# Kernel tuning notes

Measured on AMD Instinct MI355X. Metric: run time of the kernel, lower is better.

Reference implementation:

```python
import jax, jax.numpy as jnp
import numpy as np

ALPHA = 0.2  # LeakyReLU negative slope


def setup_inputs() -> dict:
    key = jax.random.key(0)
    k1, k2, k3 = jax.random.split(key, 3)
    B, N, F_IN, F_OUT = 8, 2048, 128, 64
    h = jax.random.normal(k1, (B, N, F_IN), dtype=jnp.float32)
    # nn.Linear(in, out, bias=False).weight is [out, in]; we store the transposed
    # matmul-ready form W: [F_IN, F_OUT].
    W = jax.random.normal(k2, (F_IN, F_OUT), dtype=jnp.float32) * 0.05
    # attn_fc: Linear(2*F_OUT, 1, bias=False) -> weight vector a: [2*F_OUT]
    a = jax.random.normal(k3, (2 * F_OUT,), dtype=jnp.float32) * 0.05
    return {"h": h, "W": W, "a": a}


def reference(h, W, a):
    # h: [B, N, F_in], W: [F_in, F_out], a: [2*F_out]
    F_out = W.shape[1]
    Wh = h @ W  # [B, N, F_out]
    # cat([Wh_i, Wh_j]) @ a == Wh_i @ a1 + Wh_j @ a2 -- identical math,
    # avoids materializing the [B, N, N, 2F] tensor.
    s_i = Wh @ a[:F_out]  # [B, N] contribution of row node i
    s_j = Wh @ a[F_out:]  # [B, N] contribution of col node j
    e = jax.nn.leaky_relu(s_i[:, :, None] + s_j[:, None, :], negative_slope=ALPHA)  # [B, N, N]
    attn = jax.nn.softmax(e, axis=-1)  # softmax over neighbors j
    h_prime = jnp.einsum('bij,bjf->bif', attn, Wh)  # [B, N, F_out]
    return h_prime.mean(axis=1)  # [B, F_out]
```

## Files before the change

### kernel.cpp

```cpp
#include <hip/hip_runtime.h>
#include <hip/hip_bf16.h>


#define B 8
#define N 2048
#define FIN 128
#define FOUT 64
#define ALPHA 0.2f
#define NSLICE 4
#define SLICE (N / NSLICE)
#define GSLICE 16

__global__ __launch_bounds__(256) void k2_uv(const float* __restrict__ h,
                                             const float* __restrict__ W,
                                             const float* __restrict__ a,
                                             float* __restrict__ u, float* __restrict__ v) {
    __shared__ float sw[2 * FIN];
    int t = threadIdx.x;
    if (t < FIN) {
        float wa = 0.f, wb = 0.f;
        for (int f = 0; f < FOUT; ++f) {
            float wk = W[t * FOUT + f];
            wa += wk * a[f];
            wb += wk * a[FOUT + f];
        }
        sw[t] = wa;
        sw[FIN + t] = wb;
    }
    __syncthreads();
    int wave = threadIdx.x >> 6, lane = threadIdx.x & 63;
    int node = blockIdx.x * 4 + wave;
    const float2 hx = *(const float2*)(h + (size_t)node * FIN + lane * 2);
    const float2 w1x = *(const float2*)(sw + lane * 2);
    const float2 w2x = *(const float2*)(sw + FIN + lane * 2);
    float p1 = hx.x * w1x.x + hx.y * w1x.y;
    float p2 = hx.x * w2x.x + hx.y * w2x.y;
    #pragma unroll
    for (int o = 32; o; o >>= 1) {
        p1 += __shfl_xor(p1, o);
        p2 += __shfl_xor(p2, o);
    }
    if (lane == 0) {
        u[node] = p1;
        v[node] = p2;
    }
}

__global__ __launch_bounds__(256) void k3_pass1(const float* __restrict__ u,
                                                const float* __restrict__ v,
                                                float* __restrict__ Ap, float* __restrict__ Bp) {
    __shared__ float sv[SLICE], se[SLICE], sf[SLICE];
    int b  = blockIdx.x >> 5;
    int ic = (blockIdx.x >> 2) & 7;
    int js = blockIdx.x & 3;
    int j0 = js * SLICE;
    for (int t = threadIdx.x; t < SLICE; t += 256) {
        float vj = v[b * N + j0 + t];
        sv[t] = vj;
        se[t] = expf(vj);
        sf[t] = expf(ALPHA * vj);
    }
    __syncthreads();
    int i = ic * 256 + threadIdx.x;
    float t = -u[b * N + i];
    float Ax = 0.f, Ay = 0.f, Az = 0.f, Aw = 0.f;
    float Bx = 0.f, By = 0.f, Bz = 0.f, Bw = 0.f;
    for (int j = 0; j < SLICE; j += 4) {
        float4 vv = *(const float4*)&sv[j];
        float4 ee = *(const float4*)&se[j];
        float4 ff = *(const float4*)&sf[j];
        Ax += (vv.x > t) ? ee.x : 0.f;  Bx += (vv.x > t) ? 0.f : ff.x;
        Ay += (vv.y > t) ? ee.y : 0.f;  By += (vv.y > t) ? 0.f : ff.y;
        Az += (vv.z > t) ? ee.z : 0.f;  Bz += (vv.z > t) ? 0.f : ff.z;
        Aw += (vv.w > t) ? ee.w : 0.f;  Bw += (vv.w > t) ? 0.f : ff.w;
    }
    Ap[js * (B * N) + b * N + i] = (Ax + Ay) + (Az + Aw);
    Bp[js * (B * N) + b * N + i] = (Bx + By) + (Bz + Bw);
}

__global__ __launch_bounds__(256) void k4_pass2(const float* __restrict__ u,
                                                const float* __restrict__ v,
                                                const float* __restrict__ Ap,
                                                const float* __restrict__ Bp,
                                                float* __restrict__ cp) {
    __shared__ float su[SLICE], sr1[SLICE], sr2[SLICE];
    int b  = blockIdx.x >> 5;
    int jc = (blockIdx.x >> 2) & 7;
    int is = blockIdx.x & 3;
    int i0 = is * SLICE;
    for (int t = threadIdx.x; t < SLICE; t += 256) {
        int ii = b * N + i0 + t;
        float ui = u[ii];
        float A = ((Ap[ii] + Ap[B * N + ii]) + (Ap[2 * B * N + ii] + Ap[3 * B * N + ii]));
        float Bc = ((Bp[ii] + Bp[B * N + ii]) + (Bp[2 * B * N + ii] + Bp[3 * B * N + ii]));
        float eu = expf(ui);
        float fu = expf(ALPHA * ui);
        float d = eu * A + fu * Bc;
        float inv = 1.0f / d;
        su[t] = ui;
        sr1[t] = eu * inv;
        sr2[t] = fu * inv;
    }
    __syncthreads();
    int j = jc * 256 + threadIdx.x;
    float vj = v[b * N + j];
    float t = -vj;
    float Ax = 0.f, Ay = 0.f, Az = 0.f, Aw = 0.f;
    float Bx = 0.f, By = 0.f, Bz = 0.f, Bw = 0.f;
    for (int i = 0; i < SLICE; i += 4) {
        float4 uu = *(const float4*)&su[i];
        float4 r1 = *(const float4*)&sr1[i];
        float4 r2 = *(const float4*)&sr2[i];
        Ax += (uu.x > t) ? r1.x : 0.f;  Bx += (uu.x > t) ? 0.f : r2.x;
        Ay += (uu.y > t) ? r1.y : 0.f;  By += (uu.y > t) ? 0.f : r2.y;
        Az += (uu.z > t) ? r1.z : 0.f;  Bz += (uu.z > t) ? 0.f : r2.z;
        Aw += (uu.w > t) ? r1.w : 0.f;  Bw += (uu.w > t) ? 0.f : r2.w;
    }
    float A = (Ax + Ay) + (Az + Aw);
    float Bc = (Bx + By) + (Bz + Bw);
    cp[is * (B * N) + b * N + j] = expf(vj) * A + expf(ALPHA * vj) * Bc;
}

__global__ __launch_bounds__(128) void k5_g(const float* __restrict__ h,
                                            const float* __restrict__ cp,
                                            float* __restrict__ gp) {
    int b = blockIdx.x >> 4;
    int ns = blockIdx.x & 15;
    int k = threadIdx.x;
    int n0 = ns * (N / GSLICE);
    float acc = 0.f;
    for (int n = 0; n < N / GSLICE; ++n) {
        int nn = b * N + n0 + n;
        float cn = (cp[nn] + cp[B * N + nn]) + (cp[2 * B * N + nn] + cp[3 * B * N + nn]);
        acc += cn * h[(size_t)nn * FIN + k];
    }
    gp[(size_t)blockIdx.x * FIN + k] = acc;
}

__global__ __launch_bounds__(128) void k6_out(const float* __restrict__ gp,
                                              const float* __restrict__ W,
                                              float* __restrict__ out) {
    __shared__ float sg[FIN];
    int b = blockIdx.x;
    int k = threadIdx.x;
    float g = 0.f;
    for (int s = 0; s < GSLICE; ++s) g += gp[(size_t)(b * GSLICE + s) * FIN + k];
    sg[k] = g;
    __syncthreads();
    if (k < FOUT) {
        float acc = 0.f;
        for (int kk = 0; kk < FIN; ++kk) acc += sg[kk] * W[kk * FOUT + k];
        out[b * FOUT + k] = acc * (1.0f / (float)N);
    }
}

extern "C" void kernel_launch(void* const* d_in, const int* in_sizes, int n_in,
                              void* d_out, int out_size, void* d_ws, size_t ws_size,
                              hipStream_t stream) {
    const float* h = (const float*)d_in[0];
    const float* W = (const float*)d_in[1];
    const float* a = (const float*)d_in[2];
    float* out = (float*)d_out;

    float* ws = (float*)d_ws;
    float* u   = ws;
    float* v   = u + B * N;
    float* Ap  = v + B * N;
    float* Bp  = Ap + NSLICE * B * N;
    float* cp  = Bp + NSLICE * B * N;
    float* gp  = cp + NSLICE * B * N;

    k2_uv<<<(B * N) / 4, 256, 0, stream>>>(h, W, a, u, v);
    k3_pass1<<<B * 8 * NSLICE, 256, 0, stream>>>(u, v, Ap, Bp);
    k4_pass2<<<B * 8 * NSLICE, 256, 0, stream>>>(u, v, Ap, Bp, cp);
    k5_g<<<B * GSLICE, 128, 0, stream>>>(h, cp, gp);
    k6_out<<<B, FIN, 0, stream>>>(gp, W, out);
}
```

Measured before the change: 103.4 us.

## Register-block pairwise passes over rows and parallelize W·a precompute

The two O(N²) threshold passes now give each thread 4 rows or columns (register blocking), so every shared-memory float4 load serves four accumulators. Each block covers a smaller 128-element slice across 16 slices. The W·a fold in k2 is spread over all 256 threads with shuffle reductions instead of 128 serial 64-length loops, and each block now processes 64 nodes so this prologue is repeated less often. k5 pre-reduces the 16 slice partials into shared memory once per block, and uses 32 node slices instead of 16. The trade-off is more partial-sum traffic (16 slices instead of 4) and more registers per thread.

```diff
diff --git a/kernel.cpp b/kernel.cpp
--- a/kernel.cpp
+++ b/kernel.cpp
@@ -4,78 +4,103 @@
 
 #define B 8
 #define N 2048
+#define BN (B * N)
 #define FIN 128
 #define FOUT 64
 #define ALPHA 0.2f
-#define NSLICE 4
-#define SLICE (N / NSLICE)
-#define GSLICE 16
+
+#define JS 16
+#define SJ (N / JS)
+#define IR 4
+#define GS 32
 
 __global__ __launch_bounds__(256) void k2_uv(const float* __restrict__ h,
                                              const float* __restrict__ W,
                                              const float* __restrict__ a,
                                              float* __restrict__ u, float* __restrict__ v) {
+    __shared__ float sa[2 * FOUT];
     __shared__ float sw[2 * FIN];
     int t = threadIdx.x;
-    if (t < FIN) {
-        float wa = 0.f, wb = 0.f;
-        for (int f = 0; f < FOUT; ++f) {
-            float wk = W[t * FOUT + f];
-            wa += wk * a[f];
-            wb += wk * a[FOUT + f];
-        }
-        sw[t] = wa;
-        sw[FIN + t] = wb;
-    }
-    __syncthreads();
-    int wave = threadIdx.x >> 6, lane = threadIdx.x & 63;
-    int node = blockIdx.x * 4 + wave;
-    const float2 hx = *(const float2*)(h + (size_t)node * FIN + lane * 2);
+    if (t < 2 * FOUT) sa[t] = a[t];
+    __syncthreads();
+    {
+        int kk = t >> 4;
+        int f0 = (t & 15) * 4;
+        float a1x = sa[f0], a1y = sa[f0 + 1], a1z = sa[f0 + 2], a1w = sa[f0 + 3];
+        float a2x = sa[FOUT + f0], a2y = sa[FOUT + f0 + 1], a2z = sa[FOUT + f0 + 2], a2w = sa[FOUT + f0 + 3];
+        #pragma unroll
+        for (int p = 0; p < 8; ++p) {
+            int k = p * 16 + kk;
+            float4 w4 = *(const float4*)(W + k * FOUT + f0);
+            float p1 = w4.x * a1x + w4.y * a1y + w4.z * a1z + w4.w * a1w;
+            float p2 = w4.x * a2x + w4.y * a2y + w4.z * a2z + w4.w * a2w;
+            #pragma unroll
+            for (int o = 1; o < 16; o <<= 1) {
+                p1 += __shfl_xor(p1, o);
+                p2 += __shfl_xor(p2, o);
+            }
+            if ((t & 15) == 0) { sw[k] = p1; sw[FIN + k] = p2; }
+        }
+    }
+    __syncthreads();
+    int wave = t >> 6, lane = t & 63;
     const float2 w1x = *(const float2*)(sw + lane * 2);
     const float2 w2x = *(const float2*)(sw + FIN + lane * 2);
-    float p1 = hx.x * w1x.x + hx.y * w1x.y;
-    float p2 = hx.x * w2x.x + hx.y * w2x.y;
-    #pragma unroll
-    for (int o = 32; o; o >>= 1) {
-        p1 += __shfl_xor(p1, o);
-        p2 += __shfl_xor(p2, o);
-    }
-    if (lane == 0) {
-        u[node] = p1;
-        v[node] = p2;
+    int node0 = blockIdx.x * 64 + wave * 16;
+    for (int it = 0; it < 16; ++it) {
+        int node = node0 + it;
+        const float2 hx = *(const float2*)(h + (size_t)node * FIN + lane * 2);
+        float p1 = hx.x * w1x.x + hx.y * w1x.y;
+        float p2 = hx.x * w2x.x + hx.y * w2x.y;
+        #pragma unroll
+        for (int o = 32; o; o >>= 1) {
+            p1 += __shfl_xor(p1, o);
+            p2 += __shfl_xor(p2, o);
+        }
+        if (lane == 0) { u[node] = p1; v[node] = p2; }
     }
 }
 
 __global__ __launch_bounds__(256) void k3_pass1(const float* __restrict__ u,
                                                 const float* __restrict__ v,
                                                 float* __restrict__ Ap, float* __restrict__ Bp) {
-    __shared__ float sv[SLICE], se[SLICE], sf[SLICE];
-    int b  = blockIdx.x >> 5;
-    int ic = (blockIdx.x >> 2) & 7;
-    int js = blockIdx.x & 3;
-    int j0 = js * SLICE;
-    for (int t = threadIdx.x; t < SLICE; t += 256) {
-        float vj = v[b * N + j0 + t];
+    __shared__ float sv[SJ], se[SJ], sf[SJ];
+    int bid = blockIdx.x;
+    int b = bid >> 5;
+    int ic = (bid >> 4) & 1;
+    int js = bid & 15;
+    int t = threadIdx.x;
+    if (t < SJ) {
+        float vj = v[b * N + js * SJ + t];
         sv[t] = vj;
         se[t] = expf(vj);
         sf[t] = expf(ALPHA * vj);
     }
     __syncthreads();
-    int i = ic * 256 + threadIdx.x;
-    float t = -u[b * N + i];
-    float Ax = 0.f, Ay = 0.f, Az = 0.f, Aw = 0.f;
-    float Bx = 0.f, By = 0.f, Bz = 0.f, Bw = 0.f;
-    for (int j = 0; j < SLICE; j += 4) {
+    float th[IR], A[IR], Bm[IR];
+    #pragma unroll
+    for (int r = 0; r < IR; ++r) {
+        th[r] = -u[b * N + ic * 1024 + r * 256 + t];
+        A[r] = 0.f; Bm[r] = 0.f;
+    }
+    for (int j = 0; j < SJ; j += 4) {
         float4 vv = *(const float4*)&sv[j];
         float4 ee = *(const float4*)&se[j];
         float4 ff = *(const float4*)&sf[j];
-        Ax += (vv.x > t) ? ee.x : 0.f;  Bx += (vv.x > t) ? 0.f : ff.x;
-        Ay += (vv.y > t) ? ee.y : 0.f;  By += (vv.y > t) ? 0.f : ff.y;
-        Az += (vv.z > t) ? ee.z : 0.f;  Bz += (vv.z > t) ? 0.f : ff.z;
-        Aw += (vv.w > t) ? ee.w : 0.f;  Bw += (vv.w > t) ? 0.f : ff.w;
-    }
-    Ap[js * (B * N) + b * N + i] = (Ax + Ay) + (Az + Aw);
-    Bp[js * (B * N) + b * N + i] = (Bx + By) + (Bz + Bw);
+        #pragma unroll
+        for (int r = 0; r < IR; ++r) {
+            A[r] += (vv.x > th[r]) ? ee.x : 0.f;  Bm[r] += (vv.x > th[r]) ? 0.f : ff.x;
+            A[r] += (vv.y > th[r]) ? ee.y : 0.f;  Bm[r] += (vv.y > th[r]) ? 0.f : ff.y;
+            A[r] += (vv.z > th[r]) ? ee.z : 0.f;  Bm[r] += (vv.z > th[r]) ? 0.f : ff.z;
+            A[r] += (vv.w > th[r]) ? ee.w : 0.f;  Bm[r] += (vv.w > th[r]) ? 0.f : ff.w;
+        }
+    }
+    #pragma unroll
+    for (int r = 0; r < IR; ++r) {
+        int i = ic * 1024 + r * 256 + t;
+        Ap[js * BN + b * N + i] = A[r];
+        Bp[js * BN + b * N + i] = Bm[r];
+    }
 }
 
 __global__ __launch_bounds__(256) void k4_pass2(const float* __restrict__ u,
@@ -83,58 +108,75 @@
                                                 const float* __restrict__ Ap,
                                                 const float* __restrict__ Bp,
                                                 float* __restrict__ cp) {
-    __shared__ float su[SLICE], sr1[SLICE], sr2[SLICE];
-    int b  = blockIdx.x >> 5;
-    int jc = (blockIdx.x >> 2) & 7;
-    int is = blockIdx.x & 3;
-    int i0 = is * SLICE;
-    for (int t = threadIdx.x; t < SLICE; t += 256) {
-        int ii = b * N + i0 + t;
+    __shared__ float su[SJ], sr1[SJ], sr2[SJ];
+    int bid = blockIdx.x;
+    int b = bid >> 5;
+    int jc = (bid >> 4) & 1;
+    int is = bid & 15;
+    int t = threadIdx.x;
+    if (t < SJ) {
+        int ii = b * N + is * SJ + t;
+        float A = 0.f, Bc = 0.f;
+        #pragma unroll
+        for (int s = 0; s < 16; ++s) {
+            A += Ap[s * BN + ii];
+            Bc += Bp[s * BN + ii];
+        }
         float ui = u[ii];
-        float A = ((Ap[ii] + Ap[B * N + ii]) + (Ap[2 * B * N + ii] + Ap[3 * B * N + ii]));
-        float Bc = ((Bp[ii] + Bp[B * N + ii]) + (Bp[2 * B * N + ii] + Bp[3 * B * N + ii]));
         float eu = expf(ui);
         float fu = expf(ALPHA * ui);
-        float d = eu * A + fu * Bc;
-        float inv = 1.0f / d;
+        float inv = 1.0f / (eu * A + fu * Bc);
         su[t] = ui;
         sr1[t] = eu * inv;
         sr2[t] = fu * inv;
     }
     __syncthreads();
-    int j = jc * 256 + threadIdx.x;
-    float vj = v[b * N + j];
-    float t = -vj;
-    float Ax = 0.f, Ay = 0.f, Az = 0.f, Aw = 0.f;
-    float Bx = 0.f, By = 0.f, Bz = 0.f, Bw = 0.f;
-    for (int i = 0; i < SLICE; i += 4) {
+    float vj[IR], th[IR], Cn[IR], Dn[IR];
+    #pragma unroll
+    for (int r = 0; r < IR; ++r) {
+        vj[r] = v[b * N + jc * 1024 + r * 256 + t];
+        th[r] = -vj[r];
+        Cn[r] = 0.f; Dn[r] = 0.f;
+    }
+    for (int i = 0; i < SJ; i += 4) {
         float4 uu = *(const float4*)&su[i];
         float4 r1 = *(const float4*)&sr1[i];
         float4 r2 = *(const float4*)&sr2[i];
-        Ax += (uu.x > t) ? r1.x : 0.f;  Bx += (uu.x > t) ? 0.f : r2.x;
-        Ay += (uu.y > t) ? r1.y : 0.f;  By += (uu.y > t) ? 0.f : r2.y;
-        Az += (uu.z > t) ? r1.z : 0.f;  Bz += (uu.z > t) ? 0.f : r2.z;
-        Aw += (uu.w > t) ? r1.w : 0.f;  Bw += (uu.w > t) ? 0.f : r2.w;
-    }
-    float A = (Ax + Ay) + (Az + Aw);
-    float Bc = (Bx + By) + (Bz + Bw);
-    cp[is * (B * N) + b * N + j] = expf(vj) * A + expf(ALPHA * vj) * Bc;
+        #pragma unroll
+        for (int r = 0; r < IR; ++r) {
+            Cn[r] += (uu.x > th[r]) ? r1.x : 0.f;  Dn[r] += (uu.x > th[r]) ? 0.f : r2.x;
+            Cn[r] += (uu.y > th[r]) ? r1.y : 0.f;  Dn[r] += (uu.y > th[r]) ? 0.f : r2.y;
+            Cn[r] += (uu.z > th[r]) ? r1.z : 0.f;  Dn[r] += (uu.z > th[r]) ? 0.f : r2.z;
+            Cn[r] += (uu.w > th[r]) ? r1.w : 0.f;  Dn[r] += (uu.w > th[r]) ? 0.f : r2.w;
+        }
+    }
+    #pragma unroll
+    for (int r = 0; r < IR; ++r) {
+        int j = jc * 1024 + r * 256 + t;
+        cp[is * BN + b * N + j] = expf(vj[r]) * Cn[r] + expf(ALPHA * vj[r]) * Dn[r];
+    }
 }
 
 __global__ __launch_bounds__(128) void k5_g(const float* __restrict__ h,
                                             const float* __restrict__ cp,
                                             float* __restrict__ gp) {
-    int b = blockIdx.x >> 4;
-    int ns = blockIdx.x & 15;
-    int k = threadIdx.x;
-    int n0 = ns * (N / GSLICE);
+    __shared__ float sc[64];
+    int b = blockIdx.x >> 5;
+    int ns = blockIdx.x & 31;
+    int t = threadIdx.x;
+    if (t < 64) {
+        int nn = b * N + ns * 64 + t;
+        float c = 0.f;
+        #pragma unroll
+        for (int s = 0; s < 16; ++s) c += cp[s * BN + nn];
+        sc[t] = c;
+    }
+    __syncthreads();
     float acc = 0.f;
-    for (int n = 0; n < N / GSLICE; ++n) {
-        int nn = b * N + n0 + n;
-        float cn = (cp[nn] + cp[B * N + nn]) + (cp[2 * B * N + nn] + cp[3 * B * N + nn]);
-        acc += cn * h[(size_t)nn * FIN + k];
-    }
-    gp[(size_t)blockIdx.x * FIN + k] = acc;
+    int base = b * N + ns * 64;
+    for (int n = 0; n < 64; ++n)
+        acc += sc[n] * h[(size_t)(base + n) * FIN + t];
+    gp[(size_t)blockIdx.x * FIN + t] = acc;
 }
 
 __global__ __launch_bounds__(128) void k6_out(const float* __restrict__ gp,
@@ -144,7 +186,8 @@
     int b = blockIdx.x;
     int k = threadIdx.x;
     float g = 0.f;
-    for (int s = 0; s < GSLICE; ++s) g += gp[(size_t)(b * GSLICE + s) * FIN + k];
+    #pragma unroll
+    for (int s = 0; s < GS; ++s) g += gp[(size_t)(b * GS + s) * FIN + k];
     sg[k] = g;
     __syncthreads();
     if (k < FOUT) {
@@ -163,16 +206,16 @@
     float* out = (float*)d_out;
 
     float* ws = (float*)d_ws;
-    float* u   = ws;
-    float* v   = u + B * N;
-    float* Ap  = v + B * N;
-    float* Bp  = Ap + NSLICE * B * N;
-    float* cp  = Bp + NSLICE * B * N;
-    float* gp  = cp + NSLICE * B * N;
-
-    k2_uv<<<(B * N) / 4, 256, 0, stream>>>(h, W, a, u, v);
-    k3_pass1<<<B * 8 * NSLICE, 256, 0, stream>>>(u, v, Ap, Bp);
-    k4_pass2<<<B * 8 * NSLICE, 256, 0, stream>>>(u, v, Ap, Bp, cp);
-    k5_g<<<B * GSLICE, 128, 0, stream>>>(h, cp, gp);
+    float* u  = ws;
+    float* v  = u + BN;
+    float* Ap = v + BN;
+    float* Bp = Ap + JS * BN;
+    float* cp = Bp + JS * BN;
+    float* gp = cp + JS * BN;
+
+    k2_uv<<<BN / 64, 256, 0, stream>>>(h, W, a, u, v);
+    k3_pass1<<<256, 256, 0, stream>>>(u, v, Ap, Bp);
+    k4_pass2<<<256, 256, 0, stream>>>(u, v, Ap, Bp, cp);
+    k5_g<<<256, 128, 0, stream>>>(h, cp, gp);
     k6_out<<<B, FIN, 0, stream>>>(gp, W, out);
 }
```

Result: faster. 97.20 us (-6.0%).
